# Kernel tuning notes

Hardware: AMD Instinct MI355X
Metric: run time of the kernel (lower is better)

## Reference

```python
import jax, jax.numpy as jnp
import numpy as np

N, E = 100000, 1600000
IN_DIM, HID, OUT, L = 64, 64, 10, 3
BN_EPS = 1e-5

def _bn(x, g, b):
    # BatchNorm1d training-mode forward: biased variance over the node axis
    m = jnp.mean(x, axis=0)
    v = jnp.var(x, axis=0)
    return (x - m) * jax.lax.rsqrt(v + BN_EPS) * g + b

def setup_inputs() -> dict:
    key = jax.random.key(0)
    ks = jax.random.split(key, 16)
    s_in = 1.0 / np.sqrt(IN_DIM)
    s_h = 1.0 / np.sqrt(HID)
    s_c = 1.0 / np.sqrt(HID * (L + 1))
    return {
        "x": jax.random.normal(ks[0], (N, IN_DIM), jnp.float32),
        "edge_index": jax.random.randint(ks[1], (2, E), 0, N, jnp.int32),
        "W_in": jax.random.uniform(ks[2], (IN_DIM, HID), jnp.float32, -s_in, s_in),
        "b_in": jnp.zeros((HID,), jnp.float32),
        "g_in": jnp.ones((HID,), jnp.float32),
        "be_in": jnp.zeros((HID,), jnp.float32),
        "eps": jnp.full((L,), 0.1, jnp.float32),
        "W1": jax.random.uniform(ks[3], (L, HID, HID), jnp.float32, -s_h, s_h),
        "b1": jnp.zeros((L, HID), jnp.float32),
        "g1": jnp.ones((L, HID), jnp.float32),
        "be1": jnp.zeros((L, HID), jnp.float32),
        "W2": jax.random.uniform(ks[4], (L, HID, HID), jnp.float32, -s_h, s_h),
        "b2": jnp.zeros((L, HID), jnp.float32),
        "g2": jnp.ones((L, HID), jnp.float32),
        "be2": jnp.zeros((L, HID), jnp.float32),
        "g_post": jnp.ones((L, HID), jnp.float32),
        "be_post": jnp.zeros((L, HID), jnp.float32),
        "W_out1": jax.random.uniform(ks[5], (HID * (L + 1), HID), jnp.float32, -s_c, s_c),
        "b_out1": jnp.zeros((HID,), jnp.float32),
        "g_out": jnp.ones((HID,), jnp.float32),
        "be_out": jnp.zeros((HID,), jnp.float32),
        "W_out2": jax.random.uniform(ks[6], (HID, OUT), jnp.float32, -s_h, s_h),
        "b_out2": jnp.zeros((OUT,), jnp.float32),
    }

def reference(x, edge_index, W_in, b_in, g_in, be_in, eps, W1, b1, g1, be1,
              W2, b2, g2, be2, g_post, be_post, W_out1, b_out1, g_out, be_out,
              W_out2, b_out2):
    src, dst = edge_index[0], edge_index[1]
    # input projection (dropout is identity in eval)
    h = jax.nn.relu(_bn(x @ W_in + b_in, g_in, be_in))
    layer_outputs = [h]
    for i in range(L):
        # GIN aggregation: gather neighbor feats, scatter-add to dst
        aggr = jax.ops.segment_sum(h[src], dst, num_segments=N)  # (N, HID)
        o = (1.0 + eps[i]) * h + aggr
        o = jax.nn.relu(_bn(o @ W1[i] + b1[i], g1[i], be1[i]))
        o = jax.nn.relu(_bn(o @ W2[i] + b2[i], g2[i], be2[i]))
        h = jax.nn.relu(_bn(o, g_post[i], be_post[i]))
        layer_outputs.append(h)
    h = jnp.concatenate(layer_outputs, axis=-1)  # (N, 4*HID)
    h = jax.nn.relu(_bn(h @ W_out1 + b_out1, g_out, be_out))
    return h @ W_out2 + b_out2
```

## Files before the change

### kernel.cpp

```cpp
#include <hip/hip_runtime.h>


#define HID 64
#define LAYERS 3
#define BN_EPS 1e-5f

#define BK_SHIFT 8
#define BK_MAX 512
#define PART_EPT 16

__device__ __forceinline__ float relu_aff(float x, float s, float t) {
    return fmaxf(fmaf(x, s, t), 0.f);
}

__device__ __forceinline__ void bn_fin(const float* __restrict__ raw, const float* __restrict__ g,
                                       const float* __restrict__ b, float invN, int c,
                                       float& s, float& t) {
    float m = raw[c] * invN;
    float v = fmaf(-m, m, raw[64 + c] * invN);
    float r = rsqrtf(v + BN_EPS);
    s = r * g[c];
    t = fmaf(-m, s, b[c]);
}


__global__ __launch_bounds__(256) void k_bhist(const int* __restrict__ dst, int* __restrict__ gh,
                                               int E, int nbk) {
    __shared__ int h[BK_MAX];
    for (int i = threadIdx.x; i < BK_MAX; i += 256) h[i] = 0;
    __syncthreads();
    int stride = gridDim.x * 256;
    for (int e = blockIdx.x * 256 + threadIdx.x; e < E; e += stride)
        atomicAdd(&h[dst[e] >> BK_SHIFT], 1);
    __syncthreads();
    for (int i = threadIdx.x; i < nbk; i += 256)
        if (h[i]) atomicAdd(&gh[i], h[i]);
}

__global__ __launch_bounds__(512) void k_bscan(const int* __restrict__ gh, int* __restrict__ boff,
                                               int* __restrict__ gcur, int nbk) {
    int lane = threadIdx.x & 63, wid = threadIdx.x >> 6;
    int v = (threadIdx.x < nbk) ? gh[threadIdx.x] : 0;
    int incl = v;
    for (int d = 1; d < 64; d <<= 1) { int y = __shfl_up(incl, d); if (lane >= d) incl += y; }
    __shared__ int ws[8];
    if (lane == 63) ws[wid] = incl;
    __syncthreads();
    if (threadIdx.x == 0) { int a = 0; for (int w = 0; w < 8; w++) { int t = ws[w]; ws[w] = a; a += t; } }
    __syncthreads();
    int excl = incl - v + ws[wid];
    if (threadIdx.x < nbk) { boff[threadIdx.x] = excl; gcur[threadIdx.x] = excl; }
    if (threadIdx.x == nbk - 1) boff[nbk] = excl + v;
}

__global__ __launch_bounds__(256) void k_bpart(const int* __restrict__ src, const int* __restrict__ dst,
                                               int* __restrict__ gcur, unsigned* __restrict__ pairs,
                                               int E) {
    __shared__ int h[BK_MAX], cur[BK_MAX], base[BK_MAX];
// ... 13 lines not shown
        int d = dst[e];
        int b = d >> BK_SHIFT;
        int r = atomicAdd(&cur[b], 1);
        pairs[base[b] + r] = ((unsigned)(d & ((1 << BK_SHIFT) - 1)) << 24) | (unsigned)src[e];
    }
}

__global__ __launch_bounds__(256) void k_bucket_csr(const unsigned* __restrict__ pairs,
                                                    const int* __restrict__ boff,
                                                    int* __restrict__ row_off, int* __restrict__ col,
                                                    int N, int E, int nbk) {
    int b = blockIdx.x;
    int p0 = boff[b], p1 = boff[b + 1];
    int base_node = b << BK_SHIFT;
    int nn = min(256, N - base_node);
    __shared__ int h[256], cur[256];
    h[threadIdx.x] = 0;
    __syncthreads();
    for (int p = p0 + threadIdx.x; p < p1; p += 256)
        atomicAdd(&h[pairs[p] >> 24], 1);
    __syncthreads();
    int v = h[threadIdx.x];
    int lane = threadIdx.x & 63, wid = threadIdx.x >> 6;
    int incl = v;
    for (int d = 1; d < 64; d <<= 1) { int y = __shfl_up(incl, d); if (lane >= d) incl += y; }
    __shared__ int ws[4];
    if (lane == 63) ws[wid] = incl;
    __syncthreads();
    if (threadIdx.x == 0) { int a = 0; for (int w = 0; w < 4; w++) { int t = ws[w]; ws[w] = a; a += t; } }
    __syncthreads();
    int excl = incl - v + ws[wid];
    if (threadIdx.x < nn) row_off[base_node + threadIdx.x] = p0 + excl;
    if (b == nbk - 1 && threadIdx.x == 0) row_off[N] = E;
    cur[threadIdx.x] = excl;
    __syncthreads();
    for (int p = p0 + threadIdx.x; p < p1; p += 256) {
        unsigned pk = pairs[p];
        int local = pk >> 24;
        int r = atomicAdd(&cur[local], 1);
        col[p0 + r] = (int)(pk & 0xFFFFFFu);
    }
}

__global__ __launch_bounds__(256) void k_redstats(const float* __restrict__ pst,
                                                  float* __restrict__ rawOut, int nblk) {
    int slot = blockIdx.x * 4 + (threadIdx.x >> 6);
    int lane = threadIdx.x & 63;
    float s = 0.f;
    for (int b = lane; b < nblk; b += 64) s += pst[(size_t)b * 128 + slot];
#pragma unroll
    for (int m = 1; m < 64; m <<= 1) s += __shfl_xor(s, m, 64);
    if (lane == 0) rawOut[slot] = s;
}

__global__ __launch_bounds__(256) void k_agg(const float* __restrict__ hb,
                                             const float* __restrict__ raw, const float* __restrict__ g,
                                             const float* __restrict__ b, float invN,
                                             const int* __restrict__ row_off, const int* __restrict__ col,
                                             const float* __restrict__ epsp, int li,
                                             float* __restrict__ o, int n) {
    int wid = threadIdx.x >> 6, lane = threadIdx.x & 63;
    int node = blockIdx.x * 4 + wid;
    if (node >= n) return;
    int sub = lane >> 4;
    int fc = (lane & 15) * 4;
    float s0, t0, s1, t1, s2, t2, s3, t3;
    bn_fin(raw, g, b, invN, fc + 0, s0, t0);
    bn_fin(raw, g, b, invN, fc + 1, s1, t1);
    bn_fin(raw, g, b, invN, fc + 2, s2, t2);
    bn_fin(raw, g, b, invN, fc + 3, s3, t3);
    float ax = 0.f, ay = 0.f, az = 0.f, aw = 0.f;
    int e = row_off[node], e1 = row_off[node + 1];

    while (e + 16 <= e1) {
        int i0 = col[e + sub], i1 = col[e + 4 + sub], i2 = col[e + 8 + sub], i3 = col[e + 12 + sub];
        float4 v0 = *(const float4*)&hb[(size_t)i0 * HID + fc];
        float4 v1 = *(const float4*)&hb[(size_t)i1 * HID + fc];
        float4 v2 = *(const float4*)&hb[(size_t)i2 * HID + fc];
        float4 v3 = *(const float4*)&hb[(size_t)i3 * HID + fc];
        ax += relu_aff(v0.x, s0, t0) + relu_aff(v1.x, s0, t0) + relu_aff(v2.x, s0, t0) + relu_aff(v3.x, s0, t0);
        ay += relu_aff(v0.y, s1, t1) + relu_aff(v1.y, s1, t1) + relu_aff(v2.y, s1, t1) + relu_aff(v3.y, s1, t1);
        az += relu_aff(v0.z, s2, t2) + relu_aff(v1.z, s2, t2) + relu_aff(v2.z, s2, t2) + relu_aff(v3.z, s2, t2);
        aw += relu_aff(v0.w, s3, t3) + relu_aff(v1.w, s3, t3) + relu_aff(v2.w, s3, t3) + relu_aff(v3.w, s3, t3);
        e += 16;
    }
    while (e + 4 <= e1) {
        int i = col[e + sub];
        float4 v = *(const float4*)&hb[(size_t)i * HID + fc];
        ax += relu_aff(v.x, s0, t0);
        ay += relu_aff(v.y, s1, t1);
        az += relu_aff(v.z, s2, t2);
        aw += relu_aff(v.w, s3, t3);
        e += 4;
    }
    int rem = e1 - e;
    if (sub < rem) {
        int i = col[e + sub];
        float4 v = *(const float4*)&hb[(size_t)i * HID + fc];
        ax += relu_aff(v.x, s0, t0);
        ay += relu_aff(v.y, s1, t1);
        az += relu_aff(v.z, s2, t2);
        aw += relu_aff(v.w, s3, t3);
    }
    ax += __shfl_xor(ax, 16, 64); ay += __shfl_xor(ay, 16, 64);
    az += __shfl_xor(az, 16, 64); aw += __shfl_xor(aw, 16, 64);
    ax += __shfl_xor(ax, 32, 64); ay += __shfl_xor(ay, 32, 64);
    az += __shfl_xor(az, 32, 64); aw += __shfl_xor(aw, 32, 64);
    if (sub == 0) {
        float ope = 1.f + epsp[li];
        float4 h4 = *(const float4*)&hb[(size_t)node * HID + fc];
        float4 r;
        r.x = fmaf(ope, relu_aff(h4.x, s0, t0), ax);
        r.y = fmaf(ope, relu_aff(h4.y, s1, t1), ay);
        r.z = fmaf(ope, relu_aff(h4.z, s2, t2), az);
        r.w = fmaf(ope, relu_aff(h4.w, s3, t3), aw);
        *(float4*)&o[(size_t)node * HID + fc] = r;
    }
}


#define GEMM44_COMPUTE(sAT, sW, acc, r0, c0)                                \
    _Pragma("unroll 8")                                                     \
    for (int k = 0; k < HID; k++) {                                         \
        float4 a = *(const float4*)&sAT[k * 65 + r0];                       \
        float4 w = *(const float4*)&sW[k * HID + c0];                       \
        acc[0]  = fmaf(a.x, w.x, acc[0]);  acc[1]  = fmaf(a.x, w.y, acc[1]);\
        acc[2]  = fmaf(a.x, w.z, acc[2]);  acc[3]  = fmaf(a.x, w.w, acc[3]);\
        acc[4]  = fmaf(a.y, w.x, acc[4]);  acc[5]  = fmaf(a.y, w.y, acc[5]);\
        acc[6]  = fmaf(a.y, w.z, acc[6]);  acc[7]  = fmaf(a.y, w.w, acc[7]);\
        acc[8]  = fmaf(a.z, w.x, acc[8]);  acc[9]  = fmaf(a.z, w.y, acc[9]);\
        acc[10] = fmaf(a.z, w.z, acc[10]); acc[11] = fmaf(a.z, w.w, acc[11]);\
        acc[12] = fmaf(a.w, w.x, acc[12]); acc[13] = fmaf(a.w, w.y, acc[13]);\
        acc[14] = fmaf(a.w, w.z, acc[14]); acc[15] = fmaf(a.w, w.w, acc[15]);\
    }

template <bool AFF, bool STATS>
__global__ __launch_bounds__(256) void k_gemm_t64(const float* __restrict__ A,
                                                  const float* __restrict__ raw, const float* __restrict__ g,
                                                  const float* __restrict__ b, float invN,
                                                  const float* __restrict__ W, const float* __restrict__ bias,
                                                  float* __restrict__ C, float* __restrict__ pst, int n) {
    __shared__ float stl[2 * HID];
    __shared__ float sAT[HID * 65];
    __shared__ float sW[HID * HID];
    __shared__ float ps[4][HID], pq[4][HID];
    if (AFF) {
        if (threadIdx.x < HID) {
            float s, t;
            bn_fin(raw, g, b, invN, threadIdx.x, s, t);
            stl[threadIdx.x] = s;
            stl[HID + threadIdx.x] = t;
        }
        __syncthreads();
    }
    int base = blockIdx.x * 64;
#pragma unroll
    for (int it = 0; it < 4; it++) {
        int idx = it * 256 + threadIdx.x;
        *(float4*)&sW[idx * 4] = *(const float4*)&W[idx * 4];
    }
#pragma unroll
    for (int it = 0; it < 4; it++) {
        int idx = it * 256 + threadIdx.x;
        int r = idx >> 4;
        int kc = (idx & 15) * 4;
        float4 v = make_float4(0.f, 0.f, 0.f, 0.f);
        if (base + r < n) {
            v = *(const float4*)&A[(size_t)(base + r) * HID + kc];
            if (AFF) {
                v.x = relu_aff(v.x, stl[kc + 0], stl[HID + kc + 0]);
                v.y = relu_aff(v.y, stl[kc + 1], stl[HID + kc + 1]);
                v.z = relu_aff(v.z, stl[kc + 2], stl[HID + kc + 2]);
                v.w = relu_aff(v.w, stl[kc + 3], stl[HID + kc + 3]);
            }
        }
        sAT[(kc + 0) * 65 + r] = v.x;
        sAT[(kc + 1) * 65 + r] = v.y;
        sAT[(kc + 2) * 65 + r] = v.z;
        sAT[(kc + 3) * 65 + r] = v.w;
    }
    __syncthreads();

    int c0 = (threadIdx.x & 15) * 4;
    int r0 = (threadIdx.x >> 4) * 4;
    float acc[16];
#pragma unroll
    for (int j = 0; j < 16; j++) acc[j] = 0.f;
    GEMM44_COMPUTE(sAT, sW, acc, r0, c0)

    float4 bs = *(const float4*)&bias[c0];
    float sc0 = 0.f, sc1 = 0.f, sc2 = 0.f, sc3 = 0.f;
    float qc0 = 0.f, qc1 = 0.f, qc2 = 0.f, qc3 = 0.f;
#pragma unroll
    for (int ri = 0; ri < 4; ri++) {
        int row = base + r0 + ri;
        if (row < n) {
            float4 v;
            v.x = acc[ri * 4 + 0] + bs.x;
            v.y = acc[ri * 4 + 1] + bs.y;
            v.z = acc[ri * 4 + 2] + bs.z;
            v.w = acc[ri * 4 + 3] + bs.w;
            *(float4*)&C[(size_t)row * HID + c0] = v;
            if (STATS) {
                sc0 += v.x; qc0 = fmaf(v.x, v.x, qc0);
                sc1 += v.y; qc1 = fmaf(v.y, v.y, qc1);
                sc2 += v.z; qc2 = fmaf(v.z, v.z, qc2);
                sc3 += v.w; qc3 = fmaf(v.w, v.w, qc3);
            }
        }
    }
    if (STATS) {
        int lane = threadIdx.x & 63, wv = threadIdx.x >> 6;
        sc0 += __shfl_xor(sc0, 16, 64); sc0 += __shfl_xor(sc0, 32, 64);
        sc1 += __shfl_xor(sc1, 16, 64); sc1 += __shfl_xor(sc1, 32, 64);
        sc2 += __shfl_xor(sc2, 16, 64); sc2 += __shfl_xor(sc2, 32, 64);
        sc3 += __shfl_xor(sc3, 16, 64); sc3 += __shfl_xor(sc3, 32, 64);
        qc0 += __shfl_xor(qc0, 16, 64); qc0 += __shfl_xor(qc0, 32, 64);
        qc1 += __shfl_xor(qc1, 16, 64); qc1 += __shfl_xor(qc1, 32, 64);
        qc2 += __shfl_xor(qc2, 16, 64); qc2 += __shfl_xor(qc2, 32, 64);
        qc3 += __shfl_xor(qc3, 16, 64); qc3 += __shfl_xor(qc3, 32, 64);
        if (lane < 16) {
            *(float4*)&ps[wv][c0] = make_float4(sc0, sc1, sc2, sc3);
            *(float4*)&pq[wv][c0] = make_float4(qc0, qc1, qc2, qc3);
        }
        __syncthreads();
        if (threadIdx.x < 64) {
            float s = ps[0][threadIdx.x] + ps[1][threadIdx.x] + ps[2][threadIdx.x] + ps[3][threadIdx.x];
            float q = pq[0][threadIdx.x] + pq[1][threadIdx.x] + pq[2][threadIdx.x] + pq[3][threadIdx.x];
            pst[(size_t)blockIdx.x * 128 + threadIdx.x] = s;
            pst[(size_t)blockIdx.x * 128 + 64 + threadIdx.x] = q;
        }
    }
}

__global__ __launch_bounds__(256) void k_gemm_out1_t(const float* __restrict__ B0, const float* __restrict__ B1,
                                                     const float* __restrict__ B2, const float* __restrict__ B3,
                                                     const float* __restrict__ R0, const float* __restrict__ R1,
                                                     const float* __restrict__ R2, const float* __restrict__ R3,
                                                     const float* __restrict__ G0, const float* __restrict__ G1,
                                                     const float* __restrict__ G2, const float* __restrict__ G3,
                                                     const float* __restrict__ E0, const float* __restrict__ E1,
                                                     const float* __restrict__ E2, const float* __restrict__ E3,
                                                     float invN,
                                                     const float* __restrict__ W, const float* __restrict__ bias,
                                                     float* __restrict__ C, float* __restrict__ pst, int n) {
    __shared__ float stl[4][2 * HID];
    __shared__ float sAT[HID * 65];
    __shared__ float sW[HID * HID];
    __shared__ float ps[4][HID], pq[4][HID];
    {
        int p = threadIdx.x >> 6, c = threadIdx.x & 63;
        const float* rp[4] = {R0, R1, R2, R3};
        const float* gp[4] = {G0, G1, G2, G3};
        const float* ep[4] = {E0, E1, E2, E3};
        float s, t;
        bn_fin(rp[p], gp[p], ep[p], invN, c, s, t);
        stl[p][c] = s;
        stl[p][HID + c] = t;
    }
    __syncthreads();

    int base = blockIdx.x * 64;
    int c0 = (threadIdx.x & 15) * 4;
    int r0 = (threadIdx.x >> 4) * 4;
    float acc[16];
#pragma unroll
    for (int j = 0; j < 16; j++) acc[j] = 0.f;
    const float* bufs[4] = {B0, B1, B2, B3};
#pragma unroll
    for (int pp = 0; pp < 4; pp++) {
        if (pp) __syncthreads();
        const float* Bp = bufs[pp];
        const float* Wp = W + (size_t)pp * HID * HID;
#pragma unroll
        for (int it = 0; it < 4; it++) {
            int idx = it * 256 + threadIdx.x;
            *(float4*)&sW[idx * 4] = *(const float4*)&Wp[idx * 4];
        }
#pragma unroll
        for (int it = 0; it < 4; it++) {
            int idx = it * 256 + threadIdx.x;
            int r = idx >> 4;
            int kc = (idx & 15) * 4;
            float4 v = make_float4(0.f, 0.f, 0.f, 0.f);
            if (base + r < n) {
                v = *(const float4*)&Bp[(size_t)(base + r) * HID + kc];
                v.x = relu_aff(v.x, stl[pp][kc + 0], stl[pp][HID + kc + 0]);
                v.y = relu_aff(v.y, stl[pp][kc + 1], stl[pp][HID + kc + 1]);
                v.z = relu_aff(v.z, stl[pp][kc + 2], stl[pp][HID + kc + 2]);
                v.w = relu_aff(v.w, stl[pp][kc + 3], stl[pp][HID + kc + 3]);
            }
            sAT[(kc + 0) * 65 + r] = v.x;
            sAT[(kc + 1) * 65 + r] = v.y;
            sAT[(kc + 2) * 65 + r] = v.z;
            sAT[(kc + 3) * 65 + r] = v.w;
        }
        __syncthreads();
        GEMM44_COMPUTE(sAT, sW, acc, r0, c0)
    }

    float4 bs = *(const float4*)&bias[c0];
    float sc0 = 0.f, sc1 = 0.f, sc2 = 0.f, sc3 = 0.f;
    float qc0 = 0.f, qc1 = 0.f, qc2 = 0.f, qc3 = 0.f;
#pragma unroll
    for (int ri = 0; ri < 4; ri++) {
        int row = base + r0 + ri;
        if (row < n) {
            float4 v;
            v.x = acc[ri * 4 + 0] + bs.x;
            v.y = acc[ri * 4 + 1] + bs.y;
            v.z = acc[ri * 4 + 2] + bs.z;
            v.w = acc[ri * 4 + 3] + bs.w;
            *(float4*)&C[(size_t)row * HID + c0] = v;
            sc0 += v.x; qc0 = fmaf(v.x, v.x, qc0);
            sc1 += v.y; qc1 = fmaf(v.y, v.y, qc1);
            sc2 += v.z; qc2 = fmaf(v.z, v.z, qc2);
            sc3 += v.w; qc3 = fmaf(v.w, v.w, qc3);
        }
    }
    int lane = threadIdx.x & 63, wv = threadIdx.x >> 6;
    sc0 += __shfl_xor(sc0, 16, 64); sc0 += __shfl_xor(sc0, 32, 64);
    sc1 += __shfl_xor(sc1, 16, 64); sc1 += __shfl_xor(sc1, 32, 64);
    sc2 += __shfl_xor(sc2, 16, 64); sc2 += __shfl_xor(sc2, 32, 64);
    sc3 += __shfl_xor(sc3, 16, 64); sc3 += __shfl_xor(sc3, 32, 64);
    qc0 += __shfl_xor(qc0, 16, 64); qc0 += __shfl_xor(qc0, 32, 64);
    qc1 += __shfl_xor(qc1, 16, 64); qc1 += __shfl_xor(qc1, 32, 64);
    qc2 += __shfl_xor(qc2, 16, 64); qc2 += __shfl_xor(qc2, 32, 64);
    qc3 += __shfl_xor(qc3, 16, 64); qc3 += __shfl_xor(qc3, 32, 64);
    if (lane < 16) {
        *(float4*)&ps[wv][c0] = make_float4(sc0, sc1, sc2, sc3);
        *(float4*)&pq[wv][c0] = make_float4(qc0, qc1, qc2, qc3);
    }
    __syncthreads();
    if (threadIdx.x < 64) {
        float s = ps[0][threadIdx.x] + ps[1][threadIdx.x] + ps[2][threadIdx.x] + ps[3][threadIdx.x];
        float q = pq[0][threadIdx.x] + pq[1][threadIdx.x] + pq[2][threadIdx.x] + pq[3][threadIdx.x];
        pst[(size_t)blockIdx.x * 128 + threadIdx.x] = s;
        pst[(size_t)blockIdx.x * 128 + 64 + threadIdx.x] = q;
    }
}

__global__ __launch_bounds__(256) void k_gemm_out2_t(const float* __restrict__ A,
                                                     const float* __restrict__ raw, const float* __restrict__ g,
                                                     const float* __restrict__ b, float invN,
                                                     const float* __restrict__ W, const float* __restrict__ bias,
                                                     float* __restrict__ C, int n) {
    __shared__ float stl[2 * HID];
    if (threadIdx.x < HID) {
        float s, t;
        bn_fin(raw, g, b, invN, threadIdx.x, s, t);
        stl[threadIdx.x] = s;
        stl[HID + threadIdx.x] = t;
    }
    __syncthreads();
    int lane = threadIdx.x & 63;
    int wv = threadIdx.x >> 6;
    int k0 = __builtin_amdgcn_readfirstlane(wv * 16);
    int row = blockIdx.x * 64 + lane;
    bool valid = row < n;
    float acc[10];
#pragma unroll
    for (int j = 0; j < 10; j++) acc[j] = 0.f;
    if (valid) {
        const float4* a4 = (const float4*)(A + (size_t)row * HID + k0);
#pragma unroll
        for (int kk = 0; kk < 4; kk++) {
            float4 av = a4[kk];
            float a[4] = {av.x, av.y, av.z, av.w};
#pragma unroll
            for (int u = 0; u < 4; u++) {
                int k = k0 + kk * 4 + u;
                float xv = relu_aff(a[u], stl[k], stl[HID + k]);
#pragma unroll
                for (int j = 0; j < 10; j++) acc[j] = fmaf(xv, W[k * 10 + j], acc[j]);
            }
        }
    }
    __shared__ float part[4][64][10];
#pragma unroll
    for (int j = 0; j < 10; j++) part[wv][lane][j] = acc[j];
    __syncthreads();
    if (wv == 0 && valid) {
        float* cp = C + (size_t)row * 10;
#pragma unroll
        for (int j = 0; j < 10; j++)
            cp[j] = bias[j] + part[0][lane][j] + part[1][lane][j] + part[2][lane][j] + part[3][lane][j];
    }
}

__global__ __launch_bounds__(256) void k_affine_stats(float* __restrict__ X,
                                                      const float* __restrict__ rawIn,
                                                      const float* __restrict__ g, const float* __restrict__ b,
// ... 27 lines not shown
    const float* x = (const float*)d_in[0];
    const int* ei = (const int*)d_in[1];
    const float* W_in = (const float*)d_in[2];
    const float* b_in = (const float*)d_in[3];
    const float* g_in = (const float*)d_in[4];
    const float* be_in = (const float*)d_in[5];
    const float* epsp = (const float*)d_in[6];
    const float* W1 = (const float*)d_in[7];
    const float* b1 = (const float*)d_in[8];
    const float* g1 = (const float*)d_in[9];
    const float* be1 = (const float*)d_in[10];
    const float* W2 = (const float*)d_in[11];
    const float* b2 = (const float*)d_in[12];
    const float* g2 = (const float*)d_in[13];
    const float* be2 = (const float*)d_in[14];
    const float* g_post = (const float*)d_in[15];
    const float* be_post = (const float*)d_in[16];
    const float* W_out1 = (const float*)d_in[17];
    const float* b_out1 = (const float*)d_in[18];
    const float* g_out = (const float*)d_in[19];
    const float* be_out = (const float*)d_in[20];
    const float* W_out2 = (const float*)d_in[21];
    const float* b_out2 = (const float*)d_in[22];

    const int N = in_sizes[0] / HID;
    const int E = in_sizes[1] / 2;
    const int* srcp = ei;
    const int* dstp = ei + E;

    const int nbk = (N + (1 << BK_SHIFT) - 1) >> BK_SHIFT;
    if (nbk > BK_MAX) return;
    if (N > (1 << 24)) return;

    size_t NODE = (size_t)N * HID;
    float* f = (float*)d_ws;
    float* pre0 = f;
    float* z0 = f + NODE;
    float* z1 = f + 2 * NODE;
    float* z2 = f + 3 * NODE;
    float* o = f + 4 * NODE;
    float* p = f + 5 * NODE;
    int* rc = (int*)(f + 6 * NODE);
    int* col = rc + (N + 1);
    int* gh = col + E;
    int* boff = gh + 512;
    int* gcur = boff + 513;
    float* raw = (float*)(gcur + 512);
    unsigned* pairs = (unsigned*)o;

    size_t need = (size_t)(6 * NODE) * 4 + ((size_t)(N + 1) + E + 1537) * 4 + (size_t)11 * 128 * 4;
    if (ws_size < need) return;

    float invN = 1.0f / (float)N;
    int gt = (N + 63) / 64;
    int pb = (E + 256 * PART_EPT - 1) / (256 * PART_EPT);

    hipMemsetAsync(gh, 0, 512 * sizeof(int), stream);

    k_bhist<<<512, 256, 0, stream>>>(dstp, gh, E, nbk);
    k_bscan<<<1, 512, 0, stream>>>(gh, boff, gcur, nbk);
    k_bpart<<<pb, 256, 0, stream>>>(srcp, dstp, gcur, pairs, E);
    k_bucket_csr<<<nbk, 256, 0, stream>>>(pairs, boff, rc, col, N, E, nbk);

    k_gemm_t64<false, true><<<gt, 256, 0, stream>>>(x, nullptr, nullptr, nullptr, invN,
                                                    W_in, b_in, pre0, o, N);
    k_redstats<<<32, 256, 0, stream>>>(o, raw, gt);

    float* zb[3] = {z0, z1, z2};
    for (int i = 0; i < LAYERS; i++) {
        int s1 = 1 + 3 * i, s2 = 2 + 3 * i, sp = 3 + 3 * i;
        const float* hb = (i == 0) ? pre0 : zb[i - 1];
        const float* rh = (i == 0) ? raw : raw + (size_t)(3 * i) * 128;
        const float* gh2 = (i == 0) ? g_in : g_post + (i - 1) * HID;
        const float* eh = (i == 0) ? be_in : be_post + (i - 1) * HID;
        k_agg<<<(N + 3) / 4, 256, 0, stream>>>(hb, rh, gh2, eh, invN, rc, col, epsp, i, o, N);
        k_gemm_t64<false, true><<<gt, 256, 0, stream>>>(o, nullptr, nullptr, nullptr, invN,
                                                        W1 + (size_t)i * HID * HID, b1 + i * HID,
                                                        p, zb[i], N);
        k_redstats<<<32, 256, 0, stream>>>(zb[i], raw + (size_t)s1 * 128, gt);
        k_gemm_t64<true, true><<<gt, 256, 0, stream>>>(p, raw + (size_t)s1 * 128, g1 + i * HID, be1 + i * HID,
                                                       invN, W2 + (size_t)i * HID * HID, b2 + i * HID,
                                                       zb[i], o, N);
        k_redstats<<<32, 256, 0, stream>>>(o, raw + (size_t)s2 * 128, gt);
        k_affine_stats<<<512, 256, 0, stream>>>(zb[i], raw + (size_t)s2 * 128, g2 + i * HID, be2 + i * HID, invN,
                                                o, (long long)NODE);
        k_redstats<<<32, 256, 0, stream>>>(o, raw + (size_t)sp * 128, 512);
    }

    k_gemm_out1_t<<<gt, 256, 0, stream>>>(pre0, z0, z1, z2,
                                          raw, raw + 3 * 128, raw + 6 * 128, raw + 9 * 128,
                                          g_in, g_post, g_post + HID, g_post + 2 * HID,
                                          be_in, be_post, be_post + HID, be_post + 2 * HID,
                                          invN, W_out1, b_out1, p, o, N);
    k_redstats<<<32, 256, 0, stream>>>(o, raw + 10 * 128, gt);
    k_gemm_out2_t<<<gt, 256, 0, stream>>>(p, raw + 10 * 128, g_out, be_out, invN,
                                          W_out2, b_out2, (float*)d_out, N);
}
```

Baseline: 721.5 us.

## Enlarge GEMM row tile to 128 with 8x4 register blocking per thread

After: 716.4 us. Within noise of the previous version (-0.7%).

```diff
diff --git a/kernel.cpp b/kernel.cpp
--- a/kernel.cpp
+++ b/kernel.cpp
@@ -4,6 +4,9 @@
 #define HID 64
 #define LAYERS 3
 #define BN_EPS 1e-5f
+
+#define TR 128
+#define PADR 132
 
 #define BK_SHIFT 8
 #define BK_MAX 512
@@ -190,19 +193,28 @@
 }
 
 
-#define GEMM44_COMPUTE(sAT, sW, acc, r0, c0)                                \
-    _Pragma("unroll 8")                                                     \
-    for (int k = 0; k < HID; k++) {                                         \
-        float4 a = *(const float4*)&sAT[k * 65 + r0];                       \
-        float4 w = *(const float4*)&sW[k * HID + c0];                       \
-        acc[0]  = fmaf(a.x, w.x, acc[0]);  acc[1]  = fmaf(a.x, w.y, acc[1]);\
-        acc[2]  = fmaf(a.x, w.z, acc[2]);  acc[3]  = fmaf(a.x, w.w, acc[3]);\
-        acc[4]  = fmaf(a.y, w.x, acc[4]);  acc[5]  = fmaf(a.y, w.y, acc[5]);\
-        acc[6]  = fmaf(a.y, w.z, acc[6]);  acc[7]  = fmaf(a.y, w.w, acc[7]);\
-        acc[8]  = fmaf(a.z, w.x, acc[8]);  acc[9]  = fmaf(a.z, w.y, acc[9]);\
-        acc[10] = fmaf(a.z, w.z, acc[10]); acc[11] = fmaf(a.z, w.w, acc[11]);\
-        acc[12] = fmaf(a.w, w.x, acc[12]); acc[13] = fmaf(a.w, w.y, acc[13]);\
-        acc[14] = fmaf(a.w, w.z, acc[14]); acc[15] = fmaf(a.w, w.w, acc[15]);\
+#define GEMM84_K(sAT, sW, acc, r0, c0)                                       \
+    _Pragma("unroll 4")                                                      \
+    for (int k = 0; k < HID; k++) {                                          \
+        float4 al = *(const float4*)&sAT[k * PADR + r0];                     \
+        float4 ah = *(const float4*)&sAT[k * PADR + r0 + 4];                 \
+        float4 w  = *(const float4*)&sW[k * HID + c0];                       \
+        acc[0]  = fmaf(al.x, w.x, acc[0]);  acc[1]  = fmaf(al.x, w.y, acc[1]); \
+        acc[2]  = fmaf(al.x, w.z, acc[2]);  acc[3]  = fmaf(al.x, w.w, acc[3]); \
+        acc[4]  = fmaf(al.y, w.x, acc[4]);  acc[5]  = fmaf(al.y, w.y, acc[5]); \
+        acc[6]  = fmaf(al.y, w.z, acc[6]);  acc[7]  = fmaf(al.y, w.w, acc[7]); \
+        acc[8]  = fmaf(al.z, w.x, acc[8]);  acc[9]  = fmaf(al.z, w.y, acc[9]); \
+        acc[10] = fmaf(al.z, w.z, acc[10]); acc[11] = fmaf(al.z, w.w, acc[11]); \
+        acc[12] = fmaf(al.w, w.x, acc[12]); acc[13] = fmaf(al.w, w.y, acc[13]); \
+        acc[14] = fmaf(al.w, w.z, acc[14]); acc[15] = fmaf(al.w, w.w, acc[15]); \
+        acc[16] = fmaf(ah.x, w.x, acc[16]); acc[17] = fmaf(ah.x, w.y, acc[17]); \
+        acc[18] = fmaf(ah.x, w.z, acc[18]); acc[19] = fmaf(ah.x, w.w, acc[19]); \
+        acc[20] = fmaf(ah.y, w.x, acc[20]); acc[21] = fmaf(ah.y, w.y, acc[21]); \
+        acc[22] = fmaf(ah.y, w.z, acc[22]); acc[23] = fmaf(ah.y, w.w, acc[23]); \
+        acc[24] = fmaf(ah.z, w.x, acc[24]); acc[25] = fmaf(ah.z, w.y, acc[25]); \
+        acc[26] = fmaf(ah.z, w.z, acc[26]); acc[27] = fmaf(ah.z, w.w, acc[27]); \
+        acc[28] = fmaf(ah.w, w.x, acc[28]); acc[29] = fmaf(ah.w, w.y, acc[29]); \
+        acc[30] = fmaf(ah.w, w.z, acc[30]); acc[31] = fmaf(ah.w, w.w, acc[31]); \
     }
 
 template <bool AFF, bool STATS>
@@ -212,7 +224,7 @@
                                                   const float* __restrict__ W, const float* __restrict__ bias,
                                                   float* __restrict__ C, float* __restrict__ pst, int n) {
     __shared__ float stl[2 * HID];
-    __shared__ float sAT[HID * 65];
+    __shared__ float sAT[HID * PADR];
     __shared__ float sW[HID * HID];
     __shared__ float ps[4][HID], pq[4][HID];
     if (AFF) {
@@ -224,14 +236,14 @@
         }
         __syncthreads();
     }
-    int base = blockIdx.x * 64;
+    int base = blockIdx.x * TR;
 #pragma unroll
     for (int it = 0; it < 4; it++) {
         int idx = it * 256 + threadIdx.x;
         *(float4*)&sW[idx * 4] = *(const float4*)&W[idx * 4];
     }
 #pragma unroll
-    for (int it = 0; it < 4; it++) {
+    for (int it = 0; it < 8; it++) {
         int idx = it * 256 + threadIdx.x;
         int r = idx >> 4;
         int kc = (idx & 15) * 4;
@@ -245,25 +257,24 @@
                 v.w = relu_aff(v.w, stl[kc + 3], stl[HID + kc + 3]);
             }
         }
-        sAT[(kc + 0) * 65 + r] = v.x;
-        sAT[(kc + 1) * 65 + r] = v.y;
-        sAT[(kc + 2) * 65 + r] = v.z;
-        sAT[(kc + 3) * 65 + r] = v.w;
+        sAT[(kc + 0) * PADR + r] = v.x;
+        sAT[(kc + 1) * PADR + r] = v.y;
+        sAT[(kc + 2) * PADR + r] = v.z;
+        sAT[(kc + 3) * PADR + r] = v.w;
     }
     __syncthreads();
 
     int c0 = (threadIdx.x & 15) * 4;
-    int r0 = (threadIdx.x >> 4) * 4;
-    float acc[16];
-#pragma unroll
-    for (int j = 0; j < 16; j++) acc[j] = 0.f;
-    GEMM44_COMPUTE(sAT, sW, acc, r0, c0)
+    int r0 = (threadIdx.x >> 4) * 8;
+    float acc[32];
+#pragma unroll
+    for (int j = 0; j < 32; j++) acc[j] = 0.f;
+    GEMM84_K(sAT, sW, acc, r0, c0)
 
     float4 bs = *(const float4*)&bias[c0];
-    float sc0 = 0.f, sc1 = 0.f, sc2 = 0.f, sc3 = 0.f;
-    float qc0 = 0.f, qc1 = 0.f, qc2 = 0.f, qc3 = 0.f;
-#pragma unroll
-    for (int ri = 0; ri < 4; ri++) {
+    float sc[4] = {0.f, 0.f, 0.f, 0.f}, sq[4] = {0.f, 0.f, 0.f, 0.f};
+#pragma unroll
+    for (int ri = 0; ri < 8; ri++) {
         int row = base + r0 + ri;
         if (row < n) {
             float4 v;
@@ -273,26 +284,23 @@
             v.w = acc[ri * 4 + 3] + bs.w;
             *(float4*)&C[(size_t)row * HID + c0] = v;
             if (STATS) {
-                sc0 += v.x; qc0 = fmaf(v.x, v.x, qc0);
-                sc1 += v.y; qc1 = fmaf(v.y, v.y, qc1);
-                sc2 += v.z; qc2 = fmaf(v.z, v.z, qc2);
-                sc3 += v.w; qc3 = fmaf(v.w, v.w, qc3);
+                sc[0] += v.x; sq[0] = fmaf(v.x, v.x, sq[0]);
+                sc[1] += v.y; sq[1] = fmaf(v.y, v.y, sq[1]);
+                sc[2] += v.z; sq[2] = fmaf(v.z, v.z, sq[2]);
+                sc[3] += v.w; sq[3] = fmaf(v.w, v.w, sq[3]);
             }
         }
     }
     if (STATS) {
         int lane = threadIdx.x & 63, wv = threadIdx.x >> 6;
-        sc0 += __shfl_xor(sc0, 16, 64); sc0 += __shfl_xor(sc0, 32, 64);
-        sc1 += __shfl_xor(sc1, 16, 64); sc1 += __shfl_xor(sc1, 32, 64);
-        sc2 += __shfl_xor(sc2, 16, 64); sc2 += __shfl_xor(sc2, 32, 64);
-        sc3 += __shfl_xor(sc3, 16, 64); sc3 += __shfl_xor(sc3, 32, 64);
-        qc0 += __shfl_xor(qc0, 16, 64); qc0 += __shfl_xor(qc0, 32, 64);
-        qc1 += __shfl_xor(qc1, 16, 64); qc1 += __shfl_xor(qc1, 32, 64);
-        qc2 += __shfl_xor(qc2, 16, 64); qc2 += __shfl_xor(qc2, 32, 64);
-        qc3 += __shfl_xor(qc3, 16, 64); qc3 += __shfl_xor(qc3, 32, 64);
+#pragma unroll
+        for (int j = 0; j < 4; j++) {
+            sc[j] += __shfl_xor(sc[j], 16, 64); sc[j] += __shfl_xor(sc[j], 32, 64);
+            sq[j] += __shfl_xor(sq[j], 16, 64); sq[j] += __shfl_xor(sq[j], 32, 64);
+        }
         if (lane < 16) {
-            *(float4*)&ps[wv][c0] = make_float4(sc0, sc1, sc2, sc3);
-            *(float4*)&pq[wv][c0] = make_float4(qc0, qc1, qc2, qc3);
+            *(float4*)&ps[wv][c0] = make_float4(sc[0], sc[1], sc[2], sc[3]);
+            *(float4*)&pq[wv][c0] = make_float4(sq[0], sq[1], sq[2], sq[3]);
         }
         __syncthreads();
         if (threadIdx.x < 64) {
@@ -316,7 +324,7 @@
                                                      const float* __restrict__ W, const float* __restrict__ bias,
                                                      float* __restrict__ C, float* __restrict__ pst, int n) {
     __shared__ float stl[4][2 * HID];
-    __shared__ float sAT[HID * 65];
+    __shared__ float sAT[HID * PADR];
     __shared__ float sW[HID * HID];
     __shared__ float ps[4][HID], pq[4][HID];
     {
@@ -331,12 +339,12 @@
     }
     __syncthreads();
 
-    int base = blockIdx.x * 64;
+    int base = blockIdx.x * TR;
     int c0 = (threadIdx.x & 15) * 4;
-    int r0 = (threadIdx.x >> 4) * 4;
-    float acc[16];
-#pragma unroll
-    for (int j = 0; j < 16; j++) acc[j] = 0.f;
+    int r0 = (threadIdx.x >> 4) * 8;
+    float acc[32];
+#pragma unroll
+    for (int j = 0; j < 32; j++) acc[j] = 0.f;
     const float* bufs[4] = {B0, B1, B2, B3};
 #pragma unroll
     for (int pp = 0; pp < 4; pp++) {
@@ -349,7 +357,7 @@
             *(float4*)&sW[idx * 4] = *(const float4*)&Wp[idx * 4];
         }
 #pragma unroll
-        for (int it = 0; it < 4; it++) {
+        for (int it = 0; it < 8; it++) {
             int idx = it * 256 + threadIdx.x;
             int r = idx >> 4;
             int kc = (idx & 15) * 4;
@@ -361,20 +369,19 @@
                 v.z = relu_aff(v.z, stl[pp][kc + 2], stl[pp][HID + kc + 2]);
                 v.w = relu_aff(v.w, stl[pp][kc + 3], stl[pp][HID + kc + 3]);
             }
-            sAT[(kc + 0) * 65 + r] = v.x;
-            sAT[(kc + 1) * 65 + r] = v.y;
-            sAT[(kc + 2) * 65 + r] = v.z;
-            sAT[(kc + 3) * 65 + r] = v.w;
+            sAT[(kc + 0) * PADR + r] = v.x;
+            sAT[(kc + 1) * PADR + r] = v.y;
+            sAT[(kc + 2) * PADR + r] = v.z;
+            sAT[(kc + 3) * PADR + r] = v.w;
         }
         __syncthreads();
-        GEMM44_COMPUTE(sAT, sW, acc, r0, c0)
+        GEMM84_K(sAT, sW, acc, r0, c0)
     }
 
     float4 bs = *(const float4*)&bias[c0];
-    float sc0 = 0.f, sc1 = 0.f, sc2 = 0.f, sc3 = 0.f;
-    float qc0 = 0.f, qc1 = 0.f, qc2 = 0.f, qc3 = 0.f;
-#pragma unroll
-    for (int ri = 0; ri < 4; ri++) {
+    float sc[4] = {0.f, 0.f, 0.f, 0.f}, sq[4] = {0.f, 0.f, 0.f, 0.f};
+#pragma unroll
+    for (int ri = 0; ri < 8; ri++) {
         int row = base + r0 + ri;
         if (row < n) {
             float4 v;
@@ -383,24 +390,21 @@
             v.z = acc[ri * 4 + 2] + bs.z;
             v.w = acc[ri * 4 + 3] + bs.w;
             *(float4*)&C[(size_t)row * HID + c0] = v;
-            sc0 += v.x; qc0 = fmaf(v.x, v.x, qc0);
-            sc1 += v.y; qc1 = fmaf(v.y, v.y, qc1);
-            sc2 += v.z; qc2 = fmaf(v.z, v.z, qc2);
-            sc3 += v.w; qc3 = fmaf(v.w, v.w, qc3);
+            sc[0] += v.x; sq[0] = fmaf(v.x, v.x, sq[0]);
+            sc[1] += v.y; sq[1] = fmaf(v.y, v.y, sq[1]);
+            sc[2] += v.z; sq[2] = fmaf(v.z, v.z, sq[2]);
+            sc[3] += v.w; sq[3] = fmaf(v.w, v.w, sq[3]);
         }
     }
     int lane = threadIdx.x & 63, wv = threadIdx.x >> 6;
-    sc0 += __shfl_xor(sc0, 16, 64); sc0 += __shfl_xor(sc0, 32, 64);
-    sc1 += __shfl_xor(sc1, 16, 64); sc1 += __shfl_xor(sc1, 32, 64);
-    sc2 += __shfl_xor(sc2, 16, 64); sc2 += __shfl_xor(sc2, 32, 64);
-    sc3 += __shfl_xor(sc3, 16, 64); sc3 += __shfl_xor(sc3, 32, 64);
-    qc0 += __shfl_xor(qc0, 16, 64); qc0 += __shfl_xor(qc0, 32, 64);
-    qc1 += __shfl_xor(qc1, 16, 64); qc1 += __shfl_xor(qc1, 32, 64);
-    qc2 += __shfl_xor(qc2, 16, 64); qc2 += __shfl_xor(qc2, 32, 64);
-    qc3 += __shfl_xor(qc3, 16, 64); qc3 += __shfl_xor(qc3, 32, 64);
+#pragma unroll
+    for (int j = 0; j < 4; j++) {
+        sc[j] += __shfl_xor(sc[j], 16, 64); sc[j] += __shfl_xor(sc[j], 32, 64);
+        sq[j] += __shfl_xor(sq[j], 16, 64); sq[j] += __shfl_xor(sq[j], 32, 64);
+    }
     if (lane < 16) {
-        *(float4*)&ps[wv][c0] = make_float4(sc0, sc1, sc2, sc3);
-        *(float4*)&pq[wv][c0] = make_float4(qc0, qc1, qc2, qc3);
+        *(float4*)&ps[wv][c0] = make_float4(sc[0], sc[1], sc[2], sc[3]);
+        *(float4*)&pq[wv][c0] = make_float4(sq[0], sq[1], sq[2], sq[3]);
     }
     __syncthreads();
     if (threadIdx.x < 64) {
@@ -542,7 +546,8 @@
     if (ws_size < need) return;
 
     float invN = 1.0f / (float)N;
-    int gt = (N + 63) / 64;
+    int gt128 = (N + TR - 1) / TR;
+    int gt64 = (N + 63) / 64;
     int pb = (E + 256 * PART_EPT - 1) / (256 * PART_EPT);
 
     hipMemsetAsync(gh, 0, 512 * sizeof(int), stream);
@@ -552,9 +557,9 @@
     k_bpart<<<pb, 256, 0, stream>>>(srcp, dstp, gcur, pairs, E);
     k_bucket_csr<<<nbk, 256, 0, stream>>>(pairs, boff, rc, col, N, E, nbk);
 
-    k_gemm_t64<false, true><<<gt, 256, 0, stream>>>(x, nullptr, nullptr, nullptr, invN,
-                                                    W_in, b_in, pre0, o, N);
-    k_redstats<<<32, 256, 0, stream>>>(o, raw, gt);
+    k_gemm_t64<false, true><<<gt128, 256, 0, stream>>>(x, nullptr, nullptr, nullptr, invN,
+                                                       W_in, b_in, pre0, o, N);
+    k_redstats<<<32, 256, 0, stream>>>(o, raw, gt128);
 
     float* zb[3] = {z0, z1, z2};
     for (int i = 0; i < LAYERS; i++) {
@@ -564,25 +569,25 @@
         const float* gh2 = (i == 0) ? g_in : g_post + (i - 1) * HID;
         const float* eh = (i == 0) ? be_in : be_post + (i - 1) * HID;
         k_agg<<<(N + 3) / 4, 256, 0, stream>>>(hb, rh, gh2, eh, invN, rc, col, epsp, i, o, N);
-        k_gemm_t64<false, true><<<gt, 256, 0, stream>>>(o, nullptr, nullptr, nullptr, invN,
-                                                        W1 + (size_t)i * HID * HID, b1 + i * HID,
-                                                        p, zb[i], N);
-        k_redstats<<<32, 256, 0, stream>>>(zb[i], raw + (size_t)s1 * 128, gt);
-        k_gemm_t64<true, true><<<gt, 256, 0, stream>>>(p, raw + (size_t)s1 * 128, g1 + i * HID, be1 + i * HID,
-                                                       invN, W2 + (size_t)i * HID * HID, b2 + i * HID,
-                                                       zb[i], o, N);
-        k_redstats<<<32, 256, 0, stream>>>(o, raw + (size_t)s2 * 128, gt);
+        k_gemm_t64<false, true><<<gt128, 256, 0, stream>>>(o, nullptr, nullptr, nullptr, invN,
+                                                           W1 + (size_t)i * HID * HID, b1 + i * HID,
+                                                           p, zb[i], N);
+        k_redstats<<<32, 256, 0, stream>>>(zb[i], raw + (size_t)s1 * 128, gt128);
+        k_gemm_t64<true, true><<<gt128, 256, 0, stream>>>(p, raw + (size_t)s1 * 128, g1 + i * HID, be1 + i * HID,
+                                                          invN, W2 + (size_t)i * HID * HID, b2 + i * HID,
+                                                          zb[i], o, N);
+        k_redstats<<<32, 256, 0, stream>>>(o, raw + (size_t)s2 * 128, gt128);
         k_affine_stats<<<512, 256, 0, stream>>>(zb[i], raw + (size_t)s2 * 128, g2 + i * HID, be2 + i * HID, invN,
                                                 o, (long long)NODE);
         k_redstats<<<32, 256, 0, stream>>>(o, raw + (size_t)sp * 128, 512);
     }
 
-    k_gemm_out1_t<<<gt, 256, 0, stream>>>(pre0, z0, z1, z2,
-                                          raw, raw + 3 * 128, raw + 6 * 128, raw + 9 * 128,
-                                          g_in, g_post, g_post + HID, g_post + 2 * HID,
-                                          be_in, be_post, be_post + HID, be_post + 2 * HID,
-                                          invN, W_out1, b_out1, p, o, N);
-    k_redstats<<<32, 256, 0, stream>>>(o, raw + 10 * 128, gt);
-    k_gemm_out2_t<<<gt, 256, 0, stream>>>(p, raw + 10 * 128, g_out, be_out, invN,
-                                          W_out2, b_out2, (float*)d_out, N);
-}
+    k_gemm_out1_t<<<gt128, 256, 0, stream>>>(pre0, z0, z1, z2,
+                                             raw, raw + 3 * 128, raw + 6 * 128, raw + 9 * 128,
+                                             g_in, g_post, g_post + HID, g_post + 2 * HID,
+                                             be_in, be_post, be_post + HID, be_post + 2 * HID,
+                                             invN, W_out1, b_out1, p, o, N);
+    k_redstats<<<32, 256, 0, stream>>>(o, raw + 10 * 128, gt128);
+    k_gemm_out2_t<<<gt64, 256, 0, stream>>>(p, raw + 10 * 128, g_out, be_out, invN,
+                                            W_out2, b_out2, (float*)d_out, N);
+}
```

## Fuse GIN neighbor aggregation into the first MLP GEMM kernel

Applied to the files above, without the earlier changes.

After: 796.2 us. +10.3%, slower.

```diff
diff --git a/kernel.cpp b/kernel.cpp
--- a/kernel.cpp
+++ b/kernel.cpp
@@ -123,72 +123,6 @@
     for (int m = 1; m < 64; m <<= 1) s += __shfl_xor(s, m, 64);
     if (lane == 0) rawOut[slot] = s;
 }
-
-__global__ __launch_bounds__(256) void k_agg(const float* __restrict__ hb,
-                                             const float* __restrict__ raw, const float* __restrict__ g,
-                                             const float* __restrict__ b, float invN,
-                                             const int* __restrict__ row_off, const int* __restrict__ col,
-                                             const float* __restrict__ epsp, int li,
-                                             float* __restrict__ o, int n) {
-    int wid = threadIdx.x >> 6, lane = threadIdx.x & 63;
-    int node = blockIdx.x * 4 + wid;
-    if (node >= n) return;
-    int sub = lane >> 4;
-    int fc = (lane & 15) * 4;
-    float s0, t0, s1, t1, s2, t2, s3, t3;
-    bn_fin(raw, g, b, invN, fc + 0, s0, t0);
-    bn_fin(raw, g, b, invN, fc + 1, s1, t1);
-    bn_fin(raw, g, b, invN, fc + 2, s2, t2);
-    bn_fin(raw, g, b, invN, fc + 3, s3, t3);
-    float ax = 0.f, ay = 0.f, az = 0.f, aw = 0.f;
-    int e = row_off[node], e1 = row_off[node + 1];
-
-    while (e + 16 <= e1) {
-        int i0 = col[e + sub], i1 = col[e + 4 + sub], i2 = col[e + 8 + sub], i3 = col[e + 12 + sub];
-        float4 v0 = *(const float4*)&hb[(size_t)i0 * HID + fc];
-        float4 v1 = *(const float4*)&hb[(size_t)i1 * HID + fc];
-        float4 v2 = *(const float4*)&hb[(size_t)i2 * HID + fc];
-        float4 v3 = *(const float4*)&hb[(size_t)i3 * HID + fc];
-        ax += relu_aff(v0.x, s0, t0) + relu_aff(v1.x, s0, t0) + relu_aff(v2.x, s0, t0) + relu_aff(v3.x, s0, t0);
-        ay += relu_aff(v0.y, s1, t1) + relu_aff(v1.y, s1, t1) + relu_aff(v2.y, s1, t1) + relu_aff(v3.y, s1, t1);
-        az += relu_aff(v0.z, s2, t2) + relu_aff(v1.z, s2, t2) + relu_aff(v2.z, s2, t2) + relu_aff(v3.z, s2, t2);
-        aw += relu_aff(v0.w, s3, t3) + relu_aff(v1.w, s3, t3) + relu_aff(v2.w, s3, t3) + relu_aff(v3.w, s3, t3);
-        e += 16;
-    }
-    while (e + 4 <= e1) {
-        int i = col[e + sub];
-        float4 v = *(const float4*)&hb[(size_t)i * HID + fc];
-        ax += relu_aff(v.x, s0, t0);
-        ay += relu_aff(v.y, s1, t1);
-        az += relu_aff(v.z, s2, t2);
-        aw += relu_aff(v.w, s3, t3);
-        e += 4;
-    }
-    int rem = e1 - e;
-    if (sub < rem) {
-        int i = col[e + sub];
-        float4 v = *(const float4*)&hb[(size_t)i * HID + fc];
-        ax += relu_aff(v.x, s0, t0);
-        ay += relu_aff(v.y, s1, t1);
-        az += relu_aff(v.z, s2, t2);
-        aw += relu_aff(v.w, s3, t3);
-    }
-    ax += __shfl_xor(ax, 16, 64); ay += __shfl_xor(ay, 16, 64);
-    az += __shfl_xor(az, 16, 64); aw += __shfl_xor(aw, 16, 64);
-    ax += __shfl_xor(ax, 32, 64); ay += __shfl_xor(ay, 32, 64);
-    az += __shfl_xor(az, 32, 64); aw += __shfl_xor(aw, 32, 64);
-    if (sub == 0) {
-        float ope = 1.f + epsp[li];
-        float4 h4 = *(const float4*)&hb[(size_t)node * HID + fc];
-        float4 r;
-        r.x = fmaf(ope, relu_aff(h4.x, s0, t0), ax);
-        r.y = fmaf(ope, relu_aff(h4.y, s1, t1), ay);
-        r.z = fmaf(ope, relu_aff(h4.z, s2, t2), az);
-        r.w = fmaf(ope, relu_aff(h4.w, s3, t3), aw);
-        *(float4*)&o[(size_t)node * HID + fc] = r;
-    }
-}
-
 
 #define GEMM44_COMPUTE(sAT, sW, acc, r0, c0)                                \
     _Pragma("unroll 8")                                                     \
@@ -203,6 +137,49 @@
         acc[10] = fmaf(a.z, w.z, acc[10]); acc[11] = fmaf(a.z, w.w, acc[11]);\
         acc[12] = fmaf(a.w, w.x, acc[12]); acc[13] = fmaf(a.w, w.y, acc[13]);\
         acc[14] = fmaf(a.w, w.z, acc[14]); acc[15] = fmaf(a.w, w.w, acc[15]);\
+    }
+
+#define GEMM44_EPILOGUE(STATS_ON)                                            \
+    {                                                                        \
+        float4 bs = *(const float4*)&bias[c0];                               \
+        float sc[4] = {0.f, 0.f, 0.f, 0.f}, sq[4] = {0.f, 0.f, 0.f, 0.f};    \
+        _Pragma("unroll")                                                    \
+        for (int ri = 0; ri < 4; ri++) {                                     \
+            int row = base + r0 + ri;                                        \
+            if (row < n) {                                                   \
+                float4 v;                                                    \
+                v.x = acc[ri * 4 + 0] + bs.x;                                \
+                v.y = acc[ri * 4 + 1] + bs.y;                                \
+                v.z = acc[ri * 4 + 2] + bs.z;                                \
+                v.w = acc[ri * 4 + 3] + bs.w;                                \
+                *(float4*)&C[(size_t)row * HID + c0] = v;                    \
+                if (STATS_ON) {                                              \
+                    sc[0] += v.x; sq[0] = fmaf(v.x, v.x, sq[0]);             \
+                    sc[1] += v.y; sq[1] = fmaf(v.y, v.y, sq[1]);             \
+                    sc[2] += v.z; sq[2] = fmaf(v.z, v.z, sq[2]);             \
+                    sc[3] += v.w; sq[3] = fmaf(v.w, v.w, sq[3]);             \
+                }                                                            \
+            }                                                                \
+        }                                                                    \
+        if (STATS_ON) {                                                      \
+            int lane = threadIdx.x & 63, wv = threadIdx.x >> 6;              \
+            _Pragma("unroll")                                                \
+            for (int j = 0; j < 4; j++) {                                    \
+                sc[j] += __shfl_xor(sc[j], 16, 64); sc[j] += __shfl_xor(sc[j], 32, 64); \
+                sq[j] += __shfl_xor(sq[j], 16, 64); sq[j] += __shfl_xor(sq[j], 32, 64); \
+            }                                                                \
+            if (lane < 16) {                                                 \
+                *(float4*)&ps[wv][c0] = make_float4(sc[0], sc[1], sc[2], sc[3]); \
+                *(float4*)&pq[wv][c0] = make_float4(sq[0], sq[1], sq[2], sq[3]); \
+            }                                                                \
+            __syncthreads();                                                 \
+            if (threadIdx.x < 64) {                                          \
+                float s = ps[0][threadIdx.x] + ps[1][threadIdx.x] + ps[2][threadIdx.x] + ps[3][threadIdx.x]; \
+                float q = pq[0][threadIdx.x] + pq[1][threadIdx.x] + pq[2][threadIdx.x] + pq[3][threadIdx.x]; \
+                pst[(size_t)blockIdx.x * 128 + threadIdx.x] = s;             \
+                pst[(size_t)blockIdx.x * 128 + 64 + threadIdx.x] = q;        \
+            }                                                                \
+        }                                                                    \
     }
 
 template <bool AFF, bool STATS>
@@ -258,50 +235,103 @@
 #pragma unroll
     for (int j = 0; j < 16; j++) acc[j] = 0.f;
     GEMM44_COMPUTE(sAT, sW, acc, r0, c0)
-
-    float4 bs = *(const float4*)&bias[c0];
-    float sc0 = 0.f, sc1 = 0.f, sc2 = 0.f, sc3 = 0.f;
-    float qc0 = 0.f, qc1 = 0.f, qc2 = 0.f, qc3 = 0.f;
-#pragma unroll
-    for (int ri = 0; ri < 4; ri++) {
-        int row = base + r0 + ri;
-        if (row < n) {
-            float4 v;
-            v.x = acc[ri * 4 + 0] + bs.x;
-            v.y = acc[ri * 4 + 1] + bs.y;
-            v.z = acc[ri * 4 + 2] + bs.z;
-            v.w = acc[ri * 4 + 3] + bs.w;
-            *(float4*)&C[(size_t)row * HID + c0] = v;
-            if (STATS) {
-                sc0 += v.x; qc0 = fmaf(v.x, v.x, qc0);
-                sc1 += v.y; qc1 = fmaf(v.y, v.y, qc1);
-                sc2 += v.z; qc2 = fmaf(v.z, v.z, qc2);
-                sc3 += v.w; qc3 = fmaf(v.w, v.w, qc3);
-            }
-        }
-    }
-    if (STATS) {
-        int lane = threadIdx.x & 63, wv = threadIdx.x >> 6;
-        sc0 += __shfl_xor(sc0, 16, 64); sc0 += __shfl_xor(sc0, 32, 64);
-        sc1 += __shfl_xor(sc1, 16, 64); sc1 += __shfl_xor(sc1, 32, 64);
-        sc2 += __shfl_xor(sc2, 16, 64); sc2 += __shfl_xor(sc2, 32, 64);
-        sc3 += __shfl_xor(sc3, 16, 64); sc3 += __shfl_xor(sc3, 32, 64);
-        qc0 += __shfl_xor(qc0, 16, 64); qc0 += __shfl_xor(qc0, 32, 64);
-        qc1 += __shfl_xor(qc1, 16, 64); qc1 += __shfl_xor(qc1, 32, 64);
-        qc2 += __shfl_xor(qc2, 16, 64); qc2 += __shfl_xor(qc2, 32, 64);
-        qc3 += __shfl_xor(qc3, 16, 64); qc3 += __shfl_xor(qc3, 32, 64);
-        if (lane < 16) {
-            *(float4*)&ps[wv][c0] = make_float4(sc0, sc1, sc2, sc3);
-            *(float4*)&pq[wv][c0] = make_float4(qc0, qc1, qc2, qc3);
-        }
-        __syncthreads();
-        if (threadIdx.x < 64) {
-            float s = ps[0][threadIdx.x] + ps[1][threadIdx.x] + ps[2][threadIdx.x] + ps[3][threadIdx.x];
-            float q = pq[0][threadIdx.x] + pq[1][threadIdx.x] + pq[2][threadIdx.x] + pq[3][threadIdx.x];
-            pst[(size_t)blockIdx.x * 128 + threadIdx.x] = s;
-            pst[(size_t)blockIdx.x * 128 + 64 + threadIdx.x] = q;
-        }
-    }
+    GEMM44_EPILOGUE(STATS)
+}
+
+__global__ __launch_bounds__(256) void k_agg_gemm(const float* __restrict__ hb,
+                                                  const float* __restrict__ rawH, const float* __restrict__ gH,
+                                                  const float* __restrict__ bH, float invN,
+                                                  const int* __restrict__ row_off, const int* __restrict__ col,
+                                                  const float* __restrict__ epsp, int li,
+                                                  const float* __restrict__ W, const float* __restrict__ bias,
+                                                  float* __restrict__ C, float* __restrict__ pst, int n) {
+    __shared__ float sAT[HID * 65];
+    __shared__ float sW[HID * HID];
+    __shared__ float ps[4][HID], pq[4][HID];
+
+    int base = blockIdx.x * 64;
+    int lane = threadIdx.x & 63, wv = threadIdx.x >> 6;
+    int sub = lane >> 4;
+    int fc = (lane & 15) * 4;
+
+#pragma unroll
+    for (int it = 0; it < 4; it++) {
+        int idx = it * 256 + threadIdx.x;
+        *(float4*)&sW[idx * 4] = *(const float4*)&W[idx * 4];
+    }
+
+    float s0, t0, s1, t1, s2, t2, s3, t3;
+    bn_fin(rawH, gH, bH, invN, fc + 0, s0, t0);
+    bn_fin(rawH, gH, bH, invN, fc + 1, s1, t1);
+    bn_fin(rawH, gH, bH, invN, fc + 2, s2, t2);
+    bn_fin(rawH, gH, bH, invN, fc + 3, s3, t3);
+    float ope = 1.f + epsp[li];
+
+    for (int ii = 0; ii < 16; ii++) {
+        int r = wv * 16 + ii;
+        int node = base + r;
+        float ax = 0.f, ay = 0.f, az = 0.f, aw = 0.f;
+        if (node < n) {
+            int e = row_off[node], e1 = row_off[node + 1];
+            while (e + 16 <= e1) {
+                int i0 = col[e + sub], i1 = col[e + 4 + sub];
+                int i2 = col[e + 8 + sub], i3 = col[e + 12 + sub];
+                float4 v0 = *(const float4*)&hb[(size_t)i0 * HID + fc];
+                float4 v1 = *(const float4*)&hb[(size_t)i1 * HID + fc];
+                float4 v2 = *(const float4*)&hb[(size_t)i2 * HID + fc];
+                float4 v3 = *(const float4*)&hb[(size_t)i3 * HID + fc];
+                ax += relu_aff(v0.x, s0, t0) + relu_aff(v1.x, s0, t0) + relu_aff(v2.x, s0, t0) + relu_aff(v3.x, s0, t0);
+                ay += relu_aff(v0.y, s1, t1) + relu_aff(v1.y, s1, t1) + relu_aff(v2.y, s1, t1) + relu_aff(v3.y, s1, t1);
+                az += relu_aff(v0.z, s2, t2) + relu_aff(v1.z, s2, t2) + relu_aff(v2.z, s2, t2) + relu_aff(v3.z, s2, t2);
+                aw += relu_aff(v0.w, s3, t3) + relu_aff(v1.w, s3, t3) + relu_aff(v2.w, s3, t3) + relu_aff(v3.w, s3, t3);
+                e += 16;
+            }
+            while (e + 4 <= e1) {
+                int i = col[e + sub];
+                float4 v = *(const float4*)&hb[(size_t)i * HID + fc];
+                ax += relu_aff(v.x, s0, t0);
+                ay += relu_aff(v.y, s1, t1);
+                az += relu_aff(v.z, s2, t2);
+                aw += relu_aff(v.w, s3, t3);
+                e += 4;
+            }
+            int rem = e1 - e;
+            if (sub < rem) {
+                int i = col[e + sub];
+                float4 v = *(const float4*)&hb[(size_t)i * HID + fc];
+                ax += relu_aff(v.x, s0, t0);
+                ay += relu_aff(v.y, s1, t1);
+                az += relu_aff(v.z, s2, t2);
+                aw += relu_aff(v.w, s3, t3);
+            }
+        }
+        ax += __shfl_xor(ax, 16, 64); ay += __shfl_xor(ay, 16, 64);
+        az += __shfl_xor(az, 16, 64); aw += __shfl_xor(aw, 16, 64);
+        ax += __shfl_xor(ax, 32, 64); ay += __shfl_xor(ay, 32, 64);
+        az += __shfl_xor(az, 32, 64); aw += __shfl_xor(aw, 32, 64);
+        if (sub == 0) {
+            if (node < n) {
+                float4 h4 = *(const float4*)&hb[(size_t)node * HID + fc];
+                ax = fmaf(ope, relu_aff(h4.x, s0, t0), ax);
+                ay = fmaf(ope, relu_aff(h4.y, s1, t1), ay);
+                az = fmaf(ope, relu_aff(h4.z, s2, t2), az);
+                aw = fmaf(ope, relu_aff(h4.w, s3, t3), aw);
+            }
+            sAT[(fc + 0) * 65 + r] = ax;
+            sAT[(fc + 1) * 65 + r] = ay;
+            sAT[(fc + 2) * 65 + r] = az;
+            sAT[(fc + 3) * 65 + r] = aw;
+        }
+    }
+    __syncthreads();
+
+    int c0 = (threadIdx.x & 15) * 4;
+    int r0 = (threadIdx.x >> 4) * 4;
+    float acc[16];
+#pragma unroll
+    for (int j = 0; j < 16; j++) acc[j] = 0.f;
+    GEMM44_COMPUTE(sAT, sW, acc, r0, c0)
+    GEMM44_EPILOGUE(true)
 }
 
 __global__ __launch_bounds__(256) void k_gemm_out1_t(const float* __restrict__ B0, const float* __restrict__ B1,
@@ -369,46 +399,7 @@
         __syncthreads();
         GEMM44_COMPUTE(sAT, sW, acc, r0, c0)
     }
-
-    float4 bs = *(const float4*)&bias[c0];
-    float sc0 = 0.f, sc1 = 0.f, sc2 = 0.f, sc3 = 0.f;
-    float qc0 = 0.f, qc1 = 0.f, qc2 = 0.f, qc3 = 0.f;
-#pragma unroll
-    for (int ri = 0; ri < 4; ri++) {
-        int row = base + r0 + ri;
-        if (row < n) {
-            float4 v;
-            v.x = acc[ri * 4 + 0] + bs.x;
-            v.y = acc[ri * 4 + 1] + bs.y;
-            v.z = acc[ri * 4 + 2] + bs.z;
-            v.w = acc[ri * 4 + 3] + bs.w;
-            *(float4*)&C[(size_t)row * HID + c0] = v;
-            sc0 += v.x; qc0 = fmaf(v.x, v.x, qc0);
-            sc1 += v.y; qc1 = fmaf(v.y, v.y, qc1);
-            sc2 += v.z; qc2 = fmaf(v.z, v.z, qc2);
-            sc3 += v.w; qc3 = fmaf(v.w, v.w, qc3);
-        }
-    }
-    int lane = threadIdx.x & 63, wv = threadIdx.x >> 6;
-    sc0 += __shfl_xor(sc0, 16, 64); sc0 += __shfl_xor(sc0, 32, 64);
-    sc1 += __shfl_xor(sc1, 16, 64); sc1 += __shfl_xor(sc1, 32, 64);
-    sc2 += __shfl_xor(sc2, 16, 64); sc2 += __shfl_xor(sc2, 32, 64);
-    sc3 += __shfl_xor(sc3, 16, 64); sc3 += __shfl_xor(sc3, 32, 64);
-    qc0 += __shfl_xor(qc0, 16, 64); qc0 += __shfl_xor(qc0, 32, 64);
-    qc1 += __shfl_xor(qc1, 16, 64); qc1 += __shfl_xor(qc1, 32, 64);
-    qc2 += __shfl_xor(qc2, 16, 64); qc2 += __shfl_xor(qc2, 32, 64);
-    qc3 += __shfl_xor(qc3, 16, 64); qc3 += __shfl_xor(qc3, 32, 64);
-    if (lane < 16) {
-        *(float4*)&ps[wv][c0] = make_float4(sc0, sc1, sc2, sc3);
-        *(float4*)&pq[wv][c0] = make_float4(qc0, qc1, qc2, qc3);
-    }
-    __syncthreads();
-    if (threadIdx.x < 64) {
-        float s = ps[0][threadIdx.x] + ps[1][threadIdx.x] + ps[2][threadIdx.x] + ps[3][threadIdx.x];
-        float q = pq[0][threadIdx.x] + pq[1][threadIdx.x] + pq[2][threadIdx.x] + pq[3][threadIdx.x];
-        pst[(size_t)blockIdx.x * 128 + threadIdx.x] = s;
-        pst[(size_t)blockIdx.x * 128 + 64 + threadIdx.x] = q;
-    }
+    GEMM44_EPILOGUE(true)
 }
 
 __global__ __launch_bounds__(256) void k_gemm_out2_t(const float* __restrict__ A,
@@ -563,10 +554,9 @@
         const float* rh = (i == 0) ? raw : raw + (size_t)(3 * i) * 128;
         const float* gh2 = (i == 0) ? g_in : g_post + (i - 1) * HID;
         const float* eh = (i == 0) ? be_in : be_post + (i - 1) * HID;
-        k_agg<<<(N + 3) / 4, 256, 0, stream>>>(hb, rh, gh2, eh, invN, rc, col, epsp, i, o, N);
-        k_gemm_t64<false, true><<<gt, 256, 0, stream>>>(o, nullptr, nullptr, nullptr, invN,
-                                                        W1 + (size_t)i * HID * HID, b1 + i * HID,
-                                                        p, zb[i], N);
+        k_agg_gemm<<<gt, 256, 0, stream>>>(hb, rh, gh2, eh, invN, rc, col, epsp, i,
+                                           W1 + (size_t)i * HID * HID, b1 + i * HID,
+                                           p, zb[i], N);
         k_redstats<<<32, 256, 0, stream>>>(zb[i], raw + (size_t)s1 * 128, gt);
         k_gemm_t64<true, true><<<gt, 256, 0, stream>>>(p, raw + (size_t)s1 * 128, g1 + i * HID, be1 + i * HID,
                                                        invN, W2 + (size_t)i * HID * HID, b2 + i * HID,
```
